# Optimization experiments

Hardware: AMD Instinct MI355X
Metric: run time of the kernel (lower is better)

Reference implementation:

```python
import jax, jax.numpy as jnp
import numpy as np

B, T = 32, 64            # batch, max caption length
E = 14                   # encoded image grid
ENC_D, DEC_D, ATT_D = 2048, 512, 512
PATCH, CH = 32, 3
FLAT = PATCH * PATCH * CH   # 3072
EMB = 256
PAD = PATCH // 2 + PATCH // 4  # 24
IMG = 512


def setup_inputs() -> dict:
    key = jax.random.key(0)
    ks = jax.random.split(key, 20)
    w = lambda k, shp: (0.02 * jax.random.normal(k, shp)).astype(jnp.float32)
    z = lambda *shp: jnp.zeros(shp, jnp.float32)
    lengths = jnp.concatenate(
        [jnp.array([[T]], jnp.int32),
         jax.random.randint(ks[4], (B - 1, 1), 1, T + 1, dtype=jnp.int32)], axis=0)
    return dict(
        encoder_out=jax.random.normal(ks[0], (B, E, E, ENC_D), jnp.float32),
        imgs=jax.random.normal(ks[1], (B, CH, IMG, IMG), jnp.float32),
        sequence=jax.random.randint(ks[2], (B, T, 2), 0, IMG - PATCH, dtype=jnp.int32),
        sequence_offset=jax.random.normal(ks[3], (B, T, 2), jnp.float32),
        caption_lengths=lengths,
        W_pe=w(ks[5], (EMB, FLAT)), b_pe=z(EMB),
        W_enc_att=w(ks[6], (ATT_D, ENC_D)), b_enc_att=z(ATT_D),
        W_dec_att=w(ks[7], (ATT_D, DEC_D)), b_dec_att=z(ATT_D),
        w_full=w(ks[8], (ATT_D,)), b_full=jnp.zeros((), jnp.float32),
        W_init_h=w(ks[9], (DEC_D, ENC_D + EMB)), b_init_h=z(DEC_D),
        W_init_c=w(ks[10], (DEC_D, ENC_D + EMB)), b_init_c=z(DEC_D),
        W_fb=w(ks[11], (ENC_D, DEC_D)), b_fb=z(ENC_D),
        W_ih=w(ks[12], (4 * DEC_D, ENC_D + EMB)), b_ih=z(4 * DEC_D),
        W_hh=w(ks[13], (4 * DEC_D, DEC_D)), b_hh=z(4 * DEC_D),
        W_fc=w(ks[14], (2, DEC_D)), b_fc=z(2),
        W_stop=w(ks[15], (1, DEC_D)), b_stop=z(1),
    )


def _extract_patches(imgs, seq):
    # imgs: [B,C,H,W] int keypoints seq: [B,T,2] (x,y); deterministic shift=0
    padded = jnp.pad(imgs, ((0, 0), (0, 0), (PAD, PAD), (PAD, PAD)))
    def one(img, kp):
        return jax.lax.dynamic_slice(img, (0, kp[1], kp[0]), (CH, PATCH, PATCH))
    return jax.vmap(lambda img, kps: jax.vmap(lambda kp: one(img, kp))(kps))(padded, seq)


def reference(encoder_out, imgs, sequence, sequence_offset, caption_lengths,
              W_pe, b_pe, W_enc_att, b_enc_att, W_dec_att, b_dec_att, w_full, b_full,
              W_init_h, b_init_h, W_init_c, b_init_c, W_fb, b_fb,
              W_ih, b_ih, W_hh, b_hh, W_fc, b_fc, W_stop, b_stop):
    lengths = caption_lengths[:, 0]
    sort_ind = jnp.argsort(-lengths)            # descending, like torch sort
    lengths = lengths[sort_ind]
    enc = encoder_out[sort_ind].reshape(B, -1, ENC_D)   # [B,P,ENC_D]
    imgs_s = imgs[sort_ind]
    seq_s = sequence[sort_ind]
    seq_off_s = sequence_offset[sort_ind]

    # patch embedding (dropout is identity in eval mode)
    patches = _extract_patches(imgs_s, seq_s).reshape(B, T, FLAT)
    emb = patches @ W_pe.T + b_pe               # [B,T,EMB]

    # init hidden state
    init_in = jnp.concatenate([enc.mean(axis=1), emb[:, 0, :]], axis=1)
    h = init_in @ W_init_h.T + b_init_h
    c = init_in @ W_init_c.T + b_init_c

    att1 = enc @ W_enc_att.T + b_enc_att        # [B,P,A] (loop-invariant)

    def step(carry, xs):
        h, c = carry
        emb_t, t = xs
        att2 = h @ W_dec_att.T + b_dec_att                       # [B,A]
        scores = jnp.einsum('bpa,a->bp', jax.nn.relu(att1 + att2[:, None, :]), w_full) + b_full
        alpha = jax.nn.softmax(scores, axis=1)                   # [B,P]
        awe = jnp.einsum('bpd,bp->bd', enc, alpha)               # [B,ENC_D]
        gate = jax.nn.sigmoid(h @ W_fb.T + b_fb)
        x = jnp.concatenate([gate * awe, emb_t], axis=1)
        gates = x @ W_ih.T + b_ih + h @ W_hh.T + b_hh
        i, f, g, o = jnp.split(gates, 4, axis=1)
        c_new = jax.nn.sigmoid(f) * c + jax.nn.sigmoid(i) * jnp.tanh(g)
        h_new = jax.nn.sigmoid(o) * jnp.tanh(c_new)
        mask = (t < lengths)[:, None]
        preds = jnp.where(mask, h_new @ W_fc.T + b_fc, 0.0)
        preds_stop = jnp.where(mask, jax.nn.sigmoid(h_new @ W_stop.T + b_stop), 0.0)
        alpha_m = jnp.where(mask, alpha, 0.0)
        h = jnp.where(mask, h_new, h)
        c = jnp.where(mask, c_new, c)
        return (h, c), (preds, preds_stop, alpha_m)

    (_, _), (P, PS, AL) = jax.lax.scan(step, (h, c), (emb.transpose(1, 0, 2), jnp.arange(T)))
    predictions = P.transpose(1, 0, 2)          # [B,T,2]
    predictions_stop = PS.transpose(1, 0, 2)    # [B,T,1]
    alphas = AL.transpose(1, 0, 2)              # [B,T,P]
    return predictions, predictions_stop, seq_off_s, lengths, alphas, sort_ind
```

## Files before the change

### kernel.cpp

```cpp
#include <hip/hip_runtime.h>

#define Bn 32
#define Tn 64
#define Pn 196
#define ENCD 2048
#define DECD 512
#define XDIM 2304

typedef unsigned short u16;
typedef __attribute__((ext_vector_type(8))) short bf16x8;
typedef __attribute__((ext_vector_type(4))) float f32x4;

#define MF(a,b,c) __builtin_amdgcn_mfma_f32_16x16x32_bf16(a,b,c,0,0,0)

static __device__ __forceinline__ u16 f2bf(float f){
  unsigned int u = __float_as_uint(f);
  unsigned int r = u + 0x7FFFu + ((u >> 16) & 1u);
  return (u16)(r >> 16);
}
static __device__ __forceinline__ float bf2f(u16 u){
  return __uint_as_float(((unsigned int)u) << 16);
}

#define O_PRED   0
#define O_STOP   4096
#define O_SEQOFF 6144
#define O_LEN    10240
#define O_ALPHA  10272
#define O_SORT   411680

#define WS_SORT    0
#define WS_LEN     32
#define WS_C       64
#define WS_PA      16448
#define WS_SCP     163904
#define WS_ENCM    215104
#define WS_EMB0    280640
#define WS_BCOMB   288832
#define US_H0      800000
#define US_H1      816384
#define US_XA      832768
#define US_EMBBF   898304
#define US_ATT1T   1422592
#define US_ENC     4830464
#define US_WAP     17675520
#define US_WIHE    20067584
#define US_WIH2    20591872
#define US_GEMB    24786176
#define US_PATCH   20591872
#define US_WPEB    26883328
#define US_WEA     27931904

__global__ void k_prep(const int* __restrict__ caplen, int* __restrict__ ws_sort,
                       int* __restrict__ ws_len, float* __restrict__ out){
  __shared__ int len[32];
  int i = threadIdx.x;
  if (i < 32) len[i] = caplen[i];
  __syncthreads();
  if (i < 32){
    int li = len[i], r = 0;
    for (int j = 0; j < 32; j++){
      int lj = len[j];
      r += (lj > li) || (lj == li && j < i);
    }
    ws_sort[r] = i;
    ws_len[r]  = li;
    out[O_LEN + r]  = (float)li;
    out[O_SORT + r] = (float)i;
  }
}

__global__ void k_seqoff(const float* __restrict__ seqoff, const int* __restrict__ ws_sort,
                         float* __restrict__ out){
  int idx = blockIdx.x*256 + threadIdx.x;
  int b = idx >> 7, r = idx & 127;
  out[O_SEQOFF + idx] = seqoff[ws_sort[b]*128 + r];
}

__global__ void k_encbf(const float* __restrict__ enc, const int* __restrict__ srt,
                        u16* __restrict__ dst){
  int m = blockIdx.x;
  int b = m / 196, p = m - b*196;
  const float* src = enc + ((size_t)srt[b]*196 + p)*ENCD;
  u16* d = dst + (size_t)m*ENCD;
  int i = threadIdx.x*8;
  float4 v0 = *(const float4*)(src + i);
  float4 v1 = *(const float4*)(src + i + 4);
  bf16x8 s;
  s[0]=(short)f2bf(v0.x); s[1]=(short)f2bf(v0.y); s[2]=(short)f2bf(v0.z); s[3]=(short)f2bf(v0.w);
  s[4]=(short)f2bf(v1.x); s[5]=(short)f2bf(v1.y); s[6]=(short)f2bf(v1.z); s[7]=(short)f2bf(v1.w);
  *(bf16x8*)(d + i) = s;
}

__global__ void k_encmean(const u16* __restrict__ encbf, float* __restrict__ encm){
  int b = blockIdx.x >> 3, dc = blockIdx.x & 7;
  int d = dc*256 + threadIdx.x;
  const u16* ep = encbf + (size_t)(b*196)*ENCD + d;
  float s = 0.f;
  #pragma unroll 4
  for (int p = 0; p < Pn; p++) s += bf2f(ep[(size_t)p*ENCD]);
  encm[b*ENCD + d] = s * (1.f/196.f);
}

__global__ void k_patch(const float* __restrict__ imgs, const int* __restrict__ seq,
                        const int* __restrict__ srt, u16* __restrict__ patches){
  int blk = blockIdx.x; int b = blk>>6, t = blk&63;
  int sb = srt[b];
  int x0 = seq[(sb*64+t)*2 + 0], y0 = seq[(sb*64+t)*2 + 1];
  const float* img = imgs + (size_t)sb*3*512*512;
  u16* dst = patches + (size_t)(b*64+t)*3072;
  for (int idx = threadIdx.x; idx < 3072; idx += 256){
    int c = idx>>10, rem = idx&1023, i = rem>>5, j = rem&31;
    int yy = y0 + i - 24, xx = x0 + j - 24;
    float v = 0.f;
    if ((unsigned)yy < 512u && (unsigned)xx < 512u) v = img[((size_t)c*512 + yy)*512 + xx];
    dst[idx] = f2bf(v);
  }
}

__global__ __launch_bounds__(256) void k_embedv3(const u16* __restrict__ patches,
    const u16* __restrict__ wpeb, const float* __restrict__ b_pe,
    u16* __restrict__ embbf, float* __restrict__ emb0){
  int mb = blockIdx.x >> 2, nb = blockIdx.x & 3;
  int m0 = mb*64;
  __shared__ u16 A[64*136];
  int tid = threadIdx.x, wv = tid>>6, lane = tid&63, lr = lane&15, lh = lane>>4;
  f32x4 acc[4];
  #pragma unroll
  for (int mt = 0; mt < 4; mt++) acc[mt] = (f32x4){0,0,0,0};
  for (int kc = 0; kc < 24; kc++){
    __syncthreads();
    {
      int row = tid>>2, seg = tid&3;
      const u16* src = patches + (size_t)(m0 + row)*3072 + kc*128 + seg*32;
      #pragma unroll
      for (int i = 0; i < 4; i++)
        *(bf16x8*)&A[row*136 + seg*32 + i*8] = *(const bf16x8*)(src + i*8);
    }
    __syncthreads();
    #pragma unroll
    for (int ki = 0; ki < 4; ki++){
      bf16x8 bv = *(const bf16x8*)&wpeb[(size_t)(nb*64 + wv*16 + lr)*3072 + kc*128 + ki*32 + lh*8];
      #pragma unroll
      for (int mt = 0; mt < 4; mt++){
        bf16x8 av = *(const bf16x8*)&A[(mt*16 + lr)*136 + ki*32 + lh*8];
        acc[mt] = MF(av, bv, acc[mt]);
      }
    }
  }
  int n = nb*64 + wv*16 + lr;
  float bias = b_pe[n];
  #pragma unroll
  for (int mt = 0; mt < 4; mt++){
    #pragma unroll
    for (int r = 0; r < 4; r++){
      int t = mt*16 + lh*4 + r;
      float val = acc[mt][r] + bias;
      embbf[(size_t)(m0 + t)*256 + n] = f2bf(val);
      if (t == 0) emb0[mb*256 + n] = val;
    }
  }
}

__global__ void k_cvt2(const float* __restrict__ Wih, const float* __restrict__ Whh,
    const float* __restrict__ Wdec, const float* __restrict__ Wfb,
    const float* __restrict__ Wfc, const float* __restrict__ Wstop,
    const float* __restrict__ Wea, const float* __restrict__ W_pe,
    const float* __restrict__ bih, const float* __restrict__ bhh,
    u16* __restrict__ WIH2, u16* __restrict__ WIHE,
    u16* __restrict__ WAP, u16* __restrict__ WEAd, u16* __restrict__ wpeb,
    float* __restrict__ bcomb){
  int blk = blockIdx.x, tid = threadIdx.x;
  if (blk < 2048){
    int r = blk, jp = (r & 511)*4 + (r >> 9);
    for (int i = tid; i < 2304; i += 256){
      u16 v = f2bf(Wih[(size_t)r*2304 + i]);
      if (i < 2048) WIH2[(size_t)jp*2048 + i] = v;
      else          WIHE[(size_t)jp*256 + (i - 2048)] = v;
    }
  } else if (blk < 6720){
    int j = blk - 2048;
    const float* src;
    if (j < 512)        src = Wdec + (size_t)j*512;
    else if (j < 2560)  src = Wfb + (size_t)(j-512)*512;
    else if (j < 4608)  src = Whh + (size_t)(j-2560)*512;
    else if (j == 4608) src = Wfc;
    else if (j == 4609) src = Wfc + 512;
    else if (j == 4610) src = Wstop;
    else src = 0;
    for (int i = tid; i < 512; i += 256)
      WAP[(size_t)j*512 + i] = src ? f2bf(src[i]) : (u16)0;
  } else if (blk < 7232){
    int r = blk - 6720;
    for (int i = tid; i < 2048; i += 256)
      WEAd[(size_t)r*2048 + i] = f2bf(Wea[(size_t)r*2048 + i]);
  } else if (blk < 7240){
    int jp = (blk - 7232)*256 + tid;
    int r = (jp & 3)*512 + (jp >> 2);
    bcomb[jp] = bih[r] + bhh[r];
  } else {
    int i = ((blk - 7240)*256 + tid)*4;
    float4 v = *(const float4*)(W_pe + i);
    wpeb[i+0] = f2bf(v.x); wpeb[i+1] = f2bf(v.y);
    wpeb[i+2] = f2bf(v.z); wpeb[i+3] = f2bf(v.w);
  }
}

__global__ __launch_bounds__(256) void k_gemb(const u16* __restrict__ embbf,
    const u16* __restrict__ WIHE, u16* __restrict__ gemb){
  int m0 = (blockIdx.x >> 3)*64, n0 = (blockIdx.x & 7)*256;
  __shared__ u16 A[64*264];
  int tid = threadIdx.x, wv = tid>>6, lane = tid&63, lr = lane&15, lh = lane>>4;
  {
    int row = tid>>2, seg = tid&3;
    const u16* src = embbf + (size_t)(m0 + row)*256 + seg*64;
    #pragma unroll
    for (int i = 0; i < 8; i++)
      *(bf16x8*)&A[row*264 + seg*64 + i*8] = *(const bf16x8*)(src + i*8);
  }
  __syncthreads();
  f32x4 acc[4][4];
  #pragma unroll
  for (int mt = 0; mt < 4; mt++)
    #pragma unroll
    for (int nt = 0; nt < 4; nt++) acc[mt][nt] = (f32x4){0,0,0,0};
  #pragma unroll
  for (int ki = 0; ki < 8; ki++){
    bf16x8 av[4];
    #pragma unroll
    for (int mt = 0; mt < 4; mt++)
      av[mt] = *(const bf16x8*)&A[(mt*16 + lr)*264 + ki*32 + lh*8];
    #pragma unroll
    for (int nt = 0; nt < 4; nt++){
      bf16x8 bv = *(const bf16x8*)&WIHE[(size_t)(n0 + wv*64 + nt*16 + lr)*256 + ki*32 + lh*8];
      #pragma unroll
      for (int mt = 0; mt < 4; mt++) acc[mt][nt] = MF(av[mt], bv, acc[mt][nt]);
    }
  }
  #pragma unroll
  for (int nt = 0; nt < 4; nt++){
    int n = n0 + wv*64 + nt*16 + lr;
    #pragma unroll
    for (int mt = 0; mt < 4; mt++)
      #pragma unroll
      for (int r = 0; r < 4; r++)
        gemb[(size_t)(m0 + mt*16 + lh*4 + r)*2048 + n] = f2bf(acc[mt][nt][r]);
  }
}

__global__ __launch_bounds__(256) void k_att1v4(const u16* __restrict__ encbf,
    const u16* __restrict__ Wea, const float* __restrict__ bea, u16* __restrict__ att1T){
  int mb = blockIdx.x >> 2, nb = blockIdx.x & 3;
  int m0 = mb*64;
  __shared__ u16 A[64*136];
  int tid = threadIdx.x, wv = tid>>6, lane = tid&63, lr = lane&15, lh = lane>>4;
  f32x4 acc[4][2];
  #pragma unroll
  for (int mt = 0; mt < 4; mt++){ acc[mt][0] = (f32x4){0,0,0,0}; acc[mt][1] = (f32x4){0,0,0,0}; }
  for (int kc = 0; kc < 16; kc++){
    __syncthreads();
    {
      int row = tid>>2, seg = tid&3;
      const u16* src = encbf + (size_t)(m0 + row)*2048 + kc*128 + seg*32;
      #pragma unroll
      for (int i = 0; i < 4; i++)
        *(bf16x8*)&A[row*136 + seg*32 + i*8] = *(const bf16x8*)(src + i*8);
    }
    __syncthreads();
    #pragma unroll
    for (int ki = 0; ki < 4; ki++){
      bf16x8 av[4];
      #pragma unroll
      for (int mt = 0; mt < 4; mt++)
        av[mt] = *(const bf16x8*)&A[(mt*16 + lr)*136 + ki*32 + lh*8];
      #pragma unroll
      for (int nt = 0; nt < 2; nt++){
        const u16* wp = Wea + (size_t)(nb*128 + wv*32 + nt*16 + lr)*2048 + kc*128 + ki*32 + lh*8;
        bf16x8 bv = *(const bf16x8*)wp;
        #pragma unroll
        for (int mt = 0; mt < 4; mt++) acc[mt][nt] = MF(av[mt], bv, acc[mt][nt]);
      }
    }
  }
  #pragma unroll
  for (int nt = 0; nt < 2; nt++){
    int n = nb*128 + wv*32 + nt*16 + lr;
    float bias = bea[n];
    #pragma unroll
    for (int mt = 0; mt < 4; mt++){
      #pragma unroll
      for (int r = 0; r < 4; r++){
        int m = m0 + mt*16 + lh*4 + r;
        int bb = m / 196, pp = m - bb*196;
        att1T[((size_t)bb*512 + n)*208 + pp] = f2bf(acc[mt][nt][r] + bias);
      }
    }
  }
}

__global__ __launch_bounds__(256) void k_initv3(const float* __restrict__ encm,
    const float* __restrict__ emb0,
    const float* __restrict__ Wh, const float* __restrict__ Wc,
    float* __restrict__ part){
  int kc = blockIdx.x >> 4, jb = blockIdx.x & 15;
  int tid = threadIdx.x, wv = tid>>6, lane = tid&63, lr = lane&15, lh = lane>>4;
  int j = jb*64 + wv*16 + lr;
  const float* wbase = (j < 512) ? (Wh + (size_t)j*XDIM) : (Wc + (size_t)(j-512)*XDIM);
  f32x4 acc0 = {0,0,0,0}, acc1 = {0,0,0,0};
  #pragma unroll 2
  for (int kk = 0; kk < 576; kk += 32){
    int k = kc*576 + kk + lh*8;
    float4 w0 = *(const float4*)(wbase + k);
    float4 w1 = *(const float4*)(wbase + k + 4);
    bf16x8 bv;
    bv[0]=(short)f2bf(w0.x); bv[1]=(short)f2bf(w0.y); bv[2]=(short)f2bf(w0.z); bv[3]=(short)f2bf(w0.w);
    bv[4]=(short)f2bf(w1.x); bv[5]=(short)f2bf(w1.y); bv[6]=(short)f2bf(w1.z); bv[7]=(short)f2bf(w1.w);
    float4 x0, x1, y0, y1;
    if (k < 2048){
      x0 = *(const float4*)(encm + (size_t)lr*2048 + k);
      x1 = *(const float4*)(encm + (size_t)lr*2048 + k + 4);
      y0 = *(const float4*)(encm + (size_t)(16+lr)*2048 + k);
      y1 = *(const float4*)(encm + (size_t)(16+lr)*2048 + k + 4);
    } else {
      int ke = k - 2048;
      x0 = *(const float4*)(emb0 + (size_t)lr*256 + ke);
      x1 = *(const float4*)(emb0 + (size_t)lr*256 + ke + 4);
      y0 = *(const float4*)(emb0 + (size_t)(16+lr)*256 + ke);
      y1 = *(const float4*)(emb0 + (size_t)(16+lr)*256 + ke + 4);
    }
    bf16x8 a0, a1;
    a0[0]=(short)f2bf(x0.x); a0[1]=(short)f2bf(x0.y); a0[2]=(short)f2bf(x0.z); a0[3]=(short)f2bf(x0.w);
    a0[4]=(short)f2bf(x1.x); a0[5]=(short)f2bf(x1.y); a0[6]=(short)f2bf(x1.z); a0[7]=(short)f2bf(x1.w);
    a1[0]=(short)f2bf(y0.x); a1[1]=(short)f2bf(y0.y); a1[2]=(short)f2bf(y0.z); a1[3]=(short)f2bf(y0.w);
    a1[4]=(short)f2bf(y1.x); a1[5]=(short)f2bf(y1.y); a1[6]=(short)f2bf(y1.z); a1[7]=(short)f2bf(y1.w);
    acc0 = MF(a0, bv, acc0);
    acc1 = MF(a1, bv, acc1);
  }
  #pragma unroll
  for (int r = 0; r < 4; ++r){
    int b0 = lh*4 + r, b1 = 16 + b0;
    part[(size_t)(kc*32 + b0)*1024 + j] = acc0[r];
    part[(size_t)(kc*32 + b1)*1024 + j] = acc1[r];
  }
}

__global__ __launch_bounds__(256) void k_initv3r(const float* __restrict__ part,
    const float* __restrict__ bh, const float* __restrict__ bc,
    u16* __restrict__ h_bf, float* __restrict__ c){
  int idx = blockIdx.x*256 + threadIdx.x;
  int b = idx >> 10, j = idx & 1023;
  float s = part[(size_t)b*1024 + j] + part[(size_t)(32+b)*1024 + j]
          + part[(size_t)(64+b)*1024 + j] + part[(size_t)(96+b)*1024 + j];
  if (j < 512) h_bf[(size_t)b*512 + j] = f2bf(s + bh[j]);
  else         c[(size_t)b*512 + (j-512)] = s + bc[j-512];
}

__global__ __launch_bounds__(256) void kAB(const u16* __restrict__ h, const u16* __restrict__ WAP,
    float* __restrict__ pA, const u16* __restrict__ att1T,
    const float* __restrict__ bdec, const float* __restrict__ wfull,
    float* __restrict__ scp, const float* __restrict__ bfc, const float* __restrict__ bstop,
    const int* __restrict__ len, float* __restrict__ out, int t){
  int blk = blockIdx.x, tid = threadIdx.x;
  if (t == 64 && blk != 64) return;
  if (blk < 65){
    __shared__ u16 HL[32*520];
    int wv = tid>>6, lane = tid&63, lr = lane&15, lh = lane>>4;
    for (int i = tid; i < 4096; i += 256){
      unsigned long long v = ((const unsigned long long*)h)[i];
      int row = i >> 7, col = (i & 127)*4;
      *(unsigned long long*)&HL[row*520 + col] = v;
    }
    __syncthreads();
    int j0 = 512 + blk*64 + wv*16;
    f32x4 acc0 = {0,0,0,0}, acc1 = {0,0,0,0};
    #pragma unroll 4
    for (int ki = 0; ki < 16; ++ki){
      bf16x8 bv = *(const bf16x8*)&WAP[(size_t)(j0+lr)*512 + ki*32 + lh*8];
      bf16x8 a0 = *(const bf16x8*)&HL[lr*520 + ki*32 + lh*8];
      bf16x8 a1 = *(const bf16x8*)&HL[(16+lr)*520 + ki*32 + lh*8];
      acc0 = MF(a0, bv, acc0);
      acc1 = MF(a1, bv, acc1);
    }
    int j = j0 + lr;
    if (j < 4608){
      #pragma unroll
      for (int r = 0; r < 4; ++r){
        pA[(size_t)(lh*4+r)*4608 + j]    = acc0[r];
        pA[(size_t)(lh*4+r+16)*4608 + j] = acc1[r];
      }
    } else if (j < 4611 && t > 0){
      int jj = j - 4608, tm1 = t - 1;
      #pragma unroll
      for (int r = 0; r < 4; ++r){
        #pragma unroll
        for (int hb = 0; hb < 2; ++hb){
          int b0 = lh*4 + r + hb*16;
          float val = hb ? acc1[r] : acc0[r];
          bool mk = tm1 < len[b0];
          if (jj < 2) out[O_PRED + ((size_t)b0*64 + tm1)*2 + jj] = mk ? val + bfc[jj] : 0.f;
          else        out[O_STOP + (size_t)b0*64 + tm1] =
                        mk ? 1.f/(1.f + expf(-(val + bstop[0]))) : 0.f;
        }
      }
    }
  } else {
    int kb = blk - 65, b = kb >> 3, ac = kb & 7;
    if (t >= len[b]) return;
    __shared__ u16 hL[512];
    __shared__ float a2s[64], wfs[64];
    if (tid < 128)
      ((unsigned long long*)hL)[tid] = ((const unsigned long long*)(h + (size_t)b*512))[tid];
    if (tid < 64) wfs[tid] = wfull[ac*64 + tid];
    __syncthreads();
    {
      int a = tid >> 2, q = tid & 3;
      const u16* wrow = WAP + (size_t)(ac*64 + a)*512 + q*128;
      const u16* hrow = hL + q*128;
      float acc = 0.f;
      #pragma unroll
      for (int i = 0; i < 16; ++i){
        bf16x8 wv8 = *(const bf16x8*)(wrow + i*8);
        bf16x8 hv8 = *(const bf16x8*)(hrow + i*8);
        #pragma unroll
        for (int e = 0; e < 8; ++e) acc += bf2f((u16)hv8[e]) * bf2f((u16)wv8[e]);
      }
      acc += __shfl_xor(acc, 1);
      acc += __shfl_xor(acc, 2);
      if (q == 0) a2s[a] = acc + bdec[ac*64 + a];
    }
    __syncthreads();
    int p = tid;
    if (p < 196){
      const u16* col = att1T + ((size_t)b*512 + ac*64)*208 + p;
      float acc = 0.f;
      #pragma unroll 8
      for (int a = 0; a < 64; ++a)
        acc += fmaxf(bf2f(col[(size_t)a*208]) + a2s[a], 0.f) * wfs[a];
      scp[(size_t)(b*8 + ac)*200 + p] = acc;
    }
  }
}

__global__ __launch_bounds__(256) void kB2(const float* __restrict__ scp,
    const float* __restrict__ pA, const u16* __restrict__ encbf,
    const float* __restrict__ bfull, const float* __restrict__ bfb,
    u16* __restrict__ xa, const int* __restrict__ len, float* __restrict__ out, int t){
  int b = blockIdx.x >> 3, dc = blockIdx.x & 7;
  int tid = threadIdx.x, wv = tid>>6, lane = tid&63;
  if (t >= len[b]){
    if (dc == 0 && tid < 196) out[O_ALPHA + ((size_t)b*64 + t)*196 + tid] = 0.f;
    return;
  }
  __shared__ float ev[200], redf[4], bcx[2];
  float s = -1e30f;
  if (tid < 196){
    s = bfull[0];
    #pragma unroll
    for (int q = 0; q < 8; ++q) s += scp[(size_t)(b*8 + q)*200 + tid];
  }
  float m = s;
  #pragma unroll
  for (int o = 32; o; o >>= 1) m = fmaxf(m, __shfl_down(m, o));
  if (lane == 0) redf[wv] = m;
  __syncthreads();
  if (tid == 0) bcx[0] = fmaxf(fmaxf(redf[0],redf[1]), fmaxf(redf[2],redf[3]));
  __syncthreads();
  float e = (tid < 196) ? expf(s - bcx[0]) : 0.f;
  if (tid < 200) ev[tid] = (tid < 196) ? e : 0.f;
  float sm = e;
  #pragma unroll
  for (int o = 32; o; o >>= 1) sm += __shfl_down(sm, o);
  __syncthreads();
  if (lane == 0) redf[wv] = sm;
  __syncthreads();
  if (tid == 0) bcx[1] = redf[0]+redf[1]+redf[2]+redf[3];
  __syncthreads();
  float ssum = bcx[1];
  int d = dc*256 + tid;
  const u16* ep = encbf + (size_t)(b*196)*ENCD + d;
  float q[8];
  #pragma unroll
  for (int j = 0; j < 8; ++j) q[j] = 0.f;
  #pragma unroll 2
  for (int p = 0; p < 192; p += 8){
    #pragma unroll
    for (int j = 0; j < 8; ++j)
      q[j] += ev[p+j]*bf2f(ep[(size_t)(p+j)*ENCD]);
  }
  #pragma unroll
  for (int j = 0; j < 4; ++j)
    q[j] += ev[192+j]*bf2f(ep[(size_t)(192+j)*ENCD]);
  float awe = (((q[0]+q[1])+(q[2]+q[3])) + ((q[4]+q[5])+(q[6]+q[7]))) / ssum;
  float gp = pA[(size_t)b*4608 + 512 + d] + bfb[d];
  float gate = 1.f/(1.f + expf(-gp));
  xa[(size_t)b*2048 + d] = f2bf(gate * awe);
  if (dc == 0 && tid < 196) out[O_ALPHA + ((size_t)b*64 + t)*196 + tid] = ev[tid]/ssum;
}

__global__ __launch_bounds__(512) void kC(const u16* __restrict__ xa,
    const u16* __restrict__ hc, u16* __restrict__ hn, float* __restrict__ c,
    const u16* __restrict__ WIH2, const float* __restrict__ pA,
    const float* __restrict__ bcomb, const u16* __restrict__ gemb,
    const int* __restrict__ len, int t){
  int tid = threadIdx.x, wv = tid>>6, lane = tid&63, lr = lane&15, lh = lane>>4;
  int jp0 = blockIdx.x*16;
  __shared__ float red[8*512];
  f32x4 acc0 = {0,0,0,0}, acc1 = {0,0,0,0};
  #pragma unroll
  for (int ks = 0; ks < 8; ++ks){
    int k = wv*256 + ks*32;
    bf16x8 a0 = *(const bf16x8*)&xa[(size_t)lr*2048 + k + lh*8];
    bf16x8 a1 = *(const bf16x8*)&xa[(size_t)(16+lr)*2048 + k + lh*8];
    bf16x8 bv = *(const bf16x8*)&WIH2[(size_t)(jp0+lr)*2048 + k + lh*8];
    acc0 = MF(a0, bv, acc0);
    acc1 = MF(a1, bv, acc1);
  }
  #pragma unroll
  for (int r = 0; r < 4; ++r){
    red[wv*512 + ((lh*4+r) << 4) + lr]    = acc0[r];
    red[wv*512 + ((16+lh*4+r) << 4) + lr] = acc1[r];
  }
  __syncthreads();
  {
    int b = tid >> 4, jl = tid & 15, e = jl & 3;
    int jp = jp0 + jl, u = jp >> 2;
    float g = 0.f;
    #pragma unroll
    for (int w = 0; w < 8; ++w) g += red[w*512 + tid];
    g += bcomb[jp] + bf2f(gemb[((size_t)b*64 + t)*2048 + jp])
       + pA[(size_t)b*4608 + 2560 + e*512 + u];
    float sv = (e == 2) ? tanhf(g) : 1.f/(1.f + expf(-g));
    float vb = __shfl_xor(sv, 1), vc = __shfl_xor(sv, 2), vd = __shfl_xor(vb, 2);
    float i_s = (e==0)?sv:(e==1)?vb:(e==2)?vc:vd;
    float f_s = (e==1)?sv:(e==0)?vb:(e==3)?vc:vd;
    float g_t = (e==2)?sv:(e==3)?vb:(e==0)?vc:vd;
    float o_s = (e==3)?sv:(e==2)?vb:(e==1)?vc:vd;
    float cold = c[(size_t)b*512 + u];
    float hold = bf2f(hc[(size_t)b*512 + u]);
    bool mk = t < len[b];
    float cn = mk ? (f_s*cold + i_s*g_t) : cold;
    float hv = mk ? (o_s * tanhf(cn)) : hold;
    if (e == 0){
      c[(size_t)b*512 + u] = cn;
      hn[(size_t)b*512 + u] = f2bf(hv);
    }
  }
}

extern "C" void kernel_launch(void* const* d_in, const int* in_sizes, int n_in,
                              void* d_out, int out_size, void* d_ws, size_t ws_size,
                              hipStream_t stream){
  (void)in_sizes; (void)n_in; (void)out_size; (void)ws_size;
  const float* enc_out   = (const float*)d_in[0];
  const float* imgs      = (const float*)d_in[1];
  const int*   seq       = (const int*)d_in[2];
  const float* seqoff    = (const float*)d_in[3];
  const int*   caplen    = (const int*)d_in[4];
  const float* W_pe      = (const float*)d_in[5];
  const float* b_pe      = (const float*)d_in[6];
  const float* W_enc_att = (const float*)d_in[7];
  const float* b_enc_att = (const float*)d_in[8];
  const float* W_dec_att = (const float*)d_in[9];
  const float* b_dec_att = (const float*)d_in[10];
  const float* w_full    = (const float*)d_in[11];
  const float* b_full    = (const float*)d_in[12];
  const float* W_init_h  = (const float*)d_in[13];
  const float* b_init_h  = (const float*)d_in[14];
  const float* W_init_c  = (const float*)d_in[15];
  const float* b_init_c  = (const float*)d_in[16];
  const float* W_fb      = (const float*)d_in[17];
  const float* b_fb      = (const float*)d_in[18];
  const float* W_ih      = (const float*)d_in[19];
  const float* b_ih      = (const float*)d_in[20];
  const float* W_hh      = (const float*)d_in[21];
  const float* b_hh      = (const float*)d_in[22];
  const float* W_fc      = (const float*)d_in[23];
  const float* b_fc      = (const float*)d_in[24];
  const float* W_stop    = (const float*)d_in[25];
  const float* b_stop    = (const float*)d_in[26];

  float* out = (float*)d_out;
  float* ws  = (float*)d_ws;
  int*   wsi = (int*)d_ws;
  u16*   us  = (u16*)d_ws;

  u16* H[2] = { us + US_H0, us + US_H1 };

  k_prep<<<1, 64, 0, stream>>>(caplen, wsi + WS_SORT, wsi + WS_LEN, out);
  k_seqoff<<<16, 256, 0, stream>>>(seqoff, wsi + WS_SORT, out);
  k_encbf<<<6272, 256, 0, stream>>>(enc_out, wsi + WS_SORT, us + US_ENC);
  k_encmean<<<256, 256, 0, stream>>>(us + US_ENC, ws + WS_ENCM);
  k_patch<<<2048, 256, 0, stream>>>(imgs, seq, wsi + WS_SORT, us + US_PATCH);
  k_cvt2<<<8008, 256, 0, stream>>>(W_ih, W_hh, W_dec_att, W_fb, W_fc, W_stop, W_enc_att, W_pe,
                                   b_ih, b_hh,
                                   us + US_WIH2, us + US_WIHE, us + US_WAP,
                                   us + US_WEA, us + US_WPEB, ws + WS_BCOMB);
  k_embedv3<<<128, 256, 0, stream>>>(us + US_PATCH, us + US_WPEB, b_pe,
                                     us + US_EMBBF, ws + WS_EMB0);
  k_att1v4<<<392, 256, 0, stream>>>(us + US_ENC, us + US_WEA, b_enc_att, us + US_ATT1T);
  k_gemb<<<256, 256, 0, stream>>>(us + US_EMBBF, us + US_WIHE, us + US_GEMB);
  k_initv3<<<64, 256, 0, stream>>>(ws + WS_ENCM, ws + WS_EMB0, W_init_h, W_init_c, ws + WS_PA);
  k_initv3r<<<128, 256, 0, stream>>>(ws + WS_PA, b_init_h, b_init_c, H[0], ws + WS_C);

  for (int t = 0; t < Tn; ++t){
    kAB<<<321, 256, 0, stream>>>(H[t & 1], us + US_WAP, ws + WS_PA, us + US_ATT1T,
                                 b_dec_att, w_full, ws + WS_SCP, b_fc, b_stop,
                                 wsi + WS_LEN, out, t);
    kB2<<<256, 256, 0, stream>>>(ws + WS_SCP, ws + WS_PA, us + US_ENC, b_full, b_fb,
                                 us + US_XA, wsi + WS_LEN, out, t);
    kC<<<128, 512, 0, stream>>>(us + US_XA, H[t & 1], H[(t + 1) & 1], ws + WS_C,
                                us + US_WIH2, ws + WS_PA, ws + WS_BCOMB, us + US_GEMB,
                                wsi + WS_LEN, t);
  }
  kAB<<<321, 256, 0, stream>>>(H[0], us + US_WAP, ws + WS_PA, us + US_ATT1T,
                               b_dec_att, w_full, ws + WS_SCP, b_fc, b_stop,
                               wsi + WS_LEN, out, 64);
}
```

Before: 1.919 ms.

## Merge prologue kernels into four dependency-staged launches

Combines the ten setup kernels (sort-gather, bf16 conversions, patch extraction, encoder mean, patch embedding, attention projection, input gate GEMM, and init h/c) into four launches. Each launch groups independent work by block index. The encoder mean now reads the fp32 encoder output directly instead of the bf16 copy, so it no longer has to wait for the conversion. The goal is less launch overhead and more concurrent work in the one-time prologue, while the 64-step recurrent loop stays unchanged. Mixing heterogeneous branches in one grid can unbalance block scheduling, and the encoder mean changes slightly numerically because it now sums fp32 rather than bf16 values.

New measurement: 1.904 ms. Within noise of the previous version (-0.8%).

```diff
diff --git a/kernel.cpp b/kernel.cpp
--- a/kernel.cpp
+++ b/kernel.cpp
@@ -70,106 +70,168 @@
   }
 }
 
-__global__ void k_seqoff(const float* __restrict__ seqoff, const int* __restrict__ ws_sort,
-                         float* __restrict__ out){
-  int idx = blockIdx.x*256 + threadIdx.x;
-  int b = idx >> 7, r = idx & 127;
-  out[O_SEQOFF + idx] = seqoff[ws_sort[b]*128 + r];
-}
-
-__global__ void k_encbf(const float* __restrict__ enc, const int* __restrict__ srt,
-                        u16* __restrict__ dst){
-  int m = blockIdx.x;
-  int b = m / 196, p = m - b*196;
-  const float* src = enc + ((size_t)srt[b]*196 + p)*ENCD;
-  u16* d = dst + (size_t)m*ENCD;
-  int i = threadIdx.x*8;
-  float4 v0 = *(const float4*)(src + i);
-  float4 v1 = *(const float4*)(src + i + 4);
-  bf16x8 s;
-  s[0]=(short)f2bf(v0.x); s[1]=(short)f2bf(v0.y); s[2]=(short)f2bf(v0.z); s[3]=(short)f2bf(v0.w);
-  s[4]=(short)f2bf(v1.x); s[5]=(short)f2bf(v1.y); s[6]=(short)f2bf(v1.z); s[7]=(short)f2bf(v1.w);
-  *(bf16x8*)(d + i) = s;
-}
-
-__global__ void k_encmean(const u16* __restrict__ encbf, float* __restrict__ encm){
-  int b = blockIdx.x >> 3, dc = blockIdx.x & 7;
-  int d = dc*256 + threadIdx.x;
-  const u16* ep = encbf + (size_t)(b*196)*ENCD + d;
-  float s = 0.f;
-  #pragma unroll 4
-  for (int p = 0; p < Pn; p++) s += bf2f(ep[(size_t)p*ENCD]);
-  encm[b*ENCD + d] = s * (1.f/196.f);
-}
-
-__global__ void k_patch(const float* __restrict__ imgs, const int* __restrict__ seq,
-                        const int* __restrict__ srt, u16* __restrict__ patches){
-  int blk = blockIdx.x; int b = blk>>6, t = blk&63;
-  int sb = srt[b];
-  int x0 = seq[(sb*64+t)*2 + 0], y0 = seq[(sb*64+t)*2 + 1];
-  const float* img = imgs + (size_t)sb*3*512*512;
-  u16* dst = patches + (size_t)(b*64+t)*3072;
-  for (int idx = threadIdx.x; idx < 3072; idx += 256){
-    int c = idx>>10, rem = idx&1023, i = rem>>5, j = rem&31;
-    int yy = y0 + i - 24, xx = x0 + j - 24;
-    float v = 0.f;
-    if ((unsigned)yy < 512u && (unsigned)xx < 512u) v = img[((size_t)c*512 + yy)*512 + xx];
-    dst[idx] = f2bf(v);
-  }
-}
-
-__global__ __launch_bounds__(256) void k_embedv3(const u16* __restrict__ patches,
+__global__ __launch_bounds__(256) void k_stageA(const float* __restrict__ enc,
+    const float* __restrict__ imgs, const int* __restrict__ seq,
+    const float* __restrict__ W_pe, const float* __restrict__ Wea,
+    const float* __restrict__ seqoff, const int* __restrict__ srt,
+    u16* __restrict__ encbf, float* __restrict__ encm, u16* __restrict__ patches,
+    u16* __restrict__ wpeb, u16* __restrict__ wead, float* __restrict__ out){
+  int blk = blockIdx.x, tid = threadIdx.x;
+  if (blk < 6272){
+    int m = blk;
+    int b = m / 196, p = m - b*196;
+    const float* src = enc + ((size_t)srt[b]*196 + p)*ENCD;
+    u16* d = encbf + (size_t)m*ENCD;
+    int i = tid*8;
+    float4 v0 = *(const float4*)(src + i);
+    float4 v1 = *(const float4*)(src + i + 4);
+    bf16x8 s;
+    s[0]=(short)f2bf(v0.x); s[1]=(short)f2bf(v0.y); s[2]=(short)f2bf(v0.z); s[3]=(short)f2bf(v0.w);
+    s[4]=(short)f2bf(v1.x); s[5]=(short)f2bf(v1.y); s[6]=(short)f2bf(v1.z); s[7]=(short)f2bf(v1.w);
+    *(bf16x8*)(d + i) = s;
+  } else if (blk < 6528){
+    int r = blk - 6272;
+    int b = r >> 3, dc = r & 7;
+    int d = dc*256 + tid;
+    const float* ep = enc + ((size_t)srt[b]*196)*ENCD + d;
+    float s = 0.f;
+    #pragma unroll 4
+    for (int p = 0; p < Pn; p++) s += ep[(size_t)p*ENCD];
+    encm[b*ENCD + d] = s * (1.f/196.f);
+  } else if (blk < 8576){
+    int r = blk - 6528;
+    int b = r>>6, t = r&63;
+    int sb = srt[b];
+    int x0 = seq[(sb*64+t)*2 + 0], y0 = seq[(sb*64+t)*2 + 1];
+    const float* img = imgs + (size_t)sb*3*512*512;
+    u16* dst = patches + (size_t)(b*64+t)*3072;
+    for (int idx = tid; idx < 3072; idx += 256){
+      int c = idx>>10, rem = idx&1023, i = rem>>5, j = rem&31;
+      int yy = y0 + i - 24, xx = x0 + j - 24;
+      float v = 0.f;
+      if ((unsigned)yy < 512u && (unsigned)xx < 512u) v = img[((size_t)c*512 + yy)*512 + xx];
+      dst[idx] = f2bf(v);
+    }
+  } else if (blk < 9344){
+    int i = ((blk - 8576)*256 + tid)*4;
+    float4 v = *(const float4*)(W_pe + i);
+    wpeb[i+0] = f2bf(v.x); wpeb[i+1] = f2bf(v.y);
+    wpeb[i+2] = f2bf(v.z); wpeb[i+3] = f2bf(v.w);
+  } else if (blk < 9856){
+    int r = blk - 9344;
+    for (int i = tid; i < 2048; i += 256)
+      wead[(size_t)r*2048 + i] = f2bf(Wea[(size_t)r*2048 + i]);
+  } else {
+    int idx = (blk - 9856)*256 + tid;
+    int b = idx >> 7, r = idx & 127;
+    out[O_SEQOFF + idx] = seqoff[srt[b]*128 + r];
+  }
+}
+
+__global__ __launch_bounds__(256) void k_stageB(const u16* __restrict__ patches,
     const u16* __restrict__ wpeb, const float* __restrict__ b_pe,
-    u16* __restrict__ embbf, float* __restrict__ emb0){
-  int mb = blockIdx.x >> 2, nb = blockIdx.x & 3;
-  int m0 = mb*64;
+    const u16* __restrict__ encbf, const u16* __restrict__ wead,
+    const float* __restrict__ bea,
+    u16* __restrict__ embbf, float* __restrict__ emb0, u16* __restrict__ att1T){
   __shared__ u16 A[64*136];
-  int tid = threadIdx.x, wv = tid>>6, lane = tid&63, lr = lane&15, lh = lane>>4;
-  f32x4 acc[4];
-  #pragma unroll
-  for (int mt = 0; mt < 4; mt++) acc[mt] = (f32x4){0,0,0,0};
-  for (int kc = 0; kc < 24; kc++){
-    __syncthreads();
-    {
-      int row = tid>>2, seg = tid&3;
-      const u16* src = patches + (size_t)(m0 + row)*3072 + kc*128 + seg*32;
-      #pragma unroll
-      for (int i = 0; i < 4; i++)
-        *(bf16x8*)&A[row*136 + seg*32 + i*8] = *(const bf16x8*)(src + i*8);
-    }
-    __syncthreads();
-    #pragma unroll
-    for (int ki = 0; ki < 4; ki++){
-      bf16x8 bv = *(const bf16x8*)&wpeb[(size_t)(nb*64 + wv*16 + lr)*3072 + kc*128 + ki*32 + lh*8];
+  int blk = blockIdx.x, tid = threadIdx.x;
+  int wv = tid>>6, lane = tid&63, lr = lane&15, lh = lane>>4;
+  if (blk < 128){
+    int mb = blk >> 2, nb = blk & 3;
+    int m0 = mb*64;
+    f32x4 acc[4];
+    #pragma unroll
+    for (int mt = 0; mt < 4; mt++) acc[mt] = (f32x4){0,0,0,0};
+    for (int kc = 0; kc < 24; kc++){
+      __syncthreads();
+      {
+        int row = tid>>2, seg = tid&3;
+        const u16* src = patches + (size_t)(m0 + row)*3072 + kc*128 + seg*32;
+        #pragma unroll
+        for (int i = 0; i < 4; i++)
+          *(bf16x8*)&A[row*136 + seg*32 + i*8] = *(const bf16x8*)(src + i*8);
+      }
+      __syncthreads();
+      #pragma unroll
+      for (int ki = 0; ki < 4; ki++){
+        bf16x8 bv = *(const bf16x8*)&wpeb[(size_t)(nb*64 + wv*16 + lr)*3072 + kc*128 + ki*32 + lh*8];
+        #pragma unroll
+        for (int mt = 0; mt < 4; mt++){
+          bf16x8 av = *(const bf16x8*)&A[(mt*16 + lr)*136 + ki*32 + lh*8];
+          acc[mt] = MF(av, bv, acc[mt]);
+        }
+      }
+    }
+    int n = nb*64 + wv*16 + lr;
+    float bias = b_pe[n];
+    #pragma unroll
+    for (int mt = 0; mt < 4; mt++){
+      #pragma unroll
+      for (int r = 0; r < 4; r++){
+        int t = mt*16 + lh*4 + r;
+        float val = acc[mt][r] + bias;
+        embbf[(size_t)(m0 + t)*256 + n] = f2bf(val);
+        if (t == 0) emb0[mb*256 + n] = val;
+      }
+    }
+  } else {
+    int ab = blk - 128;
+    int mb = ab >> 2, nb = ab & 3;
+    int m0 = mb*64;
+    f32x4 acc[4][2];
+    #pragma unroll
+    for (int mt = 0; mt < 4; mt++){ acc[mt][0] = (f32x4){0,0,0,0}; acc[mt][1] = (f32x4){0,0,0,0}; }
+    for (int kc = 0; kc < 16; kc++){
+      __syncthreads();
+      {
+        int row = tid>>2, seg = tid&3;
+        const u16* src = encbf + (size_t)(m0 + row)*2048 + kc*128 + seg*32;
+        #pragma unroll
+        for (int i = 0; i < 4; i++)
+          *(bf16x8*)&A[row*136 + seg*32 + i*8] = *(const bf16x8*)(src + i*8);
+      }
+      __syncthreads();
+      #pragma unroll
+      for (int ki = 0; ki < 4; ki++){
+        bf16x8 av[4];
+        #pragma unroll
+        for (int mt = 0; mt < 4; mt++)
+          av[mt] = *(const bf16x8*)&A[(mt*16 + lr)*136 + ki*32 + lh*8];
+        #pragma unroll
+        for (int nt = 0; nt < 2; nt++){
+          const u16* wp = wead + (size_t)(nb*128 + wv*32 + nt*16 + lr)*2048 + kc*128 + ki*32 + lh*8;
+          bf16x8 bv = *(const bf16x8*)wp;
+          #pragma unroll
+          for (int mt = 0; mt < 4; mt++) acc[mt][nt] = MF(av[mt], bv, acc[mt][nt]);
+        }
+      }
+    }
+    #pragma unroll
+    for (int nt = 0; nt < 2; nt++){
+      int n = nb*128 + wv*32 + nt*16 + lr;
+      float bias = bea[n];
       #pragma unroll
       for (int mt = 0; mt < 4; mt++){
-        bf16x8 av = *(const bf16x8*)&A[(mt*16 + lr)*136 + ki*32 + lh*8];
-        acc[mt] = MF(av, bv, acc[mt]);
-      }
-    }
-  }
-  int n = nb*64 + wv*16 + lr;
-  float bias = b_pe[n];
-  #pragma unroll
-  for (int mt = 0; mt < 4; mt++){
-    #pragma unroll
-    for (int r = 0; r < 4; r++){
-      int t = mt*16 + lh*4 + r;
-      float val = acc[mt][r] + bias;
-      embbf[(size_t)(m0 + t)*256 + n] = f2bf(val);
-      if (t == 0) emb0[mb*256 + n] = val;
-    }
-  }
-}
-
-__global__ void k_cvt2(const float* __restrict__ Wih, const float* __restrict__ Whh,
-    const float* __restrict__ Wdec, const float* __restrict__ Wfb,
-    const float* __restrict__ Wfc, const float* __restrict__ Wstop,
-    const float* __restrict__ Wea, const float* __restrict__ W_pe,
-    const float* __restrict__ bih, const float* __restrict__ bhh,
-    u16* __restrict__ WIH2, u16* __restrict__ WIHE,
-    u16* __restrict__ WAP, u16* __restrict__ WEAd, u16* __restrict__ wpeb,
-    float* __restrict__ bcomb){
+        #pragma unroll
+        for (int r = 0; r < 4; r++){
+          int m = m0 + mt*16 + lh*4 + r;
+          int bb = m / 196, pp = m - bb*196;
+          att1T[((size_t)bb*512 + n)*208 + pp] = f2bf(acc[mt][nt][r] + bias);
+        }
+      }
+    }
+  }
+}
+
+__global__ __launch_bounds__(256) void k_stageC(const float* __restrict__ Wih,
+    const float* __restrict__ Whh, const float* __restrict__ Wdec,
+    const float* __restrict__ Wfb, const float* __restrict__ Wfc,
+    const float* __restrict__ Wstop, const float* __restrict__ bih,
+    const float* __restrict__ bhh,
+    const float* __restrict__ encm, const float* __restrict__ emb0,
+    const float* __restrict__ Wh, const float* __restrict__ Wc,
+    u16* __restrict__ WIH2, u16* __restrict__ WIHE, u16* __restrict__ WAP,
+    float* __restrict__ bcomb, float* __restrict__ part){
   int blk = blockIdx.x, tid = threadIdx.x;
   if (blk < 2048){
     int r = blk, jp = (r & 511)*4 + (r >> 9);
@@ -190,169 +252,107 @@
     else src = 0;
     for (int i = tid; i < 512; i += 256)
       WAP[(size_t)j*512 + i] = src ? f2bf(src[i]) : (u16)0;
-  } else if (blk < 7232){
-    int r = blk - 6720;
-    for (int i = tid; i < 2048; i += 256)
-      WEAd[(size_t)r*2048 + i] = f2bf(Wea[(size_t)r*2048 + i]);
-  } else if (blk < 7240){
-    int jp = (blk - 7232)*256 + tid;
+  } else if (blk < 6728){
+    int jp = (blk - 6720)*256 + tid;
     int r = (jp & 3)*512 + (jp >> 2);
     bcomb[jp] = bih[r] + bhh[r];
   } else {
-    int i = ((blk - 7240)*256 + tid)*4;
-    float4 v = *(const float4*)(W_pe + i);
-    wpeb[i+0] = f2bf(v.x); wpeb[i+1] = f2bf(v.y);
-    wpeb[i+2] = f2bf(v.z); wpeb[i+3] = f2bf(v.w);
-  }
-}
-
-__global__ __launch_bounds__(256) void k_gemb(const u16* __restrict__ embbf,
-    const u16* __restrict__ WIHE, u16* __restrict__ gemb){
-  int m0 = (blockIdx.x >> 3)*64, n0 = (blockIdx.x & 7)*256;
+    int ib = blk - 6728;
+    int kc = ib >> 4, jb = ib & 15;
+    int wv = tid>>6, lane = tid&63, lr = lane&15, lh = lane>>4;
+    int j = jb*64 + wv*16 + lr;
+    const float* wbase = (j < 512) ? (Wh + (size_t)j*XDIM) : (Wc + (size_t)(j-512)*XDIM);
+    f32x4 acc0 = {0,0,0,0}, acc1 = {0,0,0,0};
+    #pragma unroll 2
+    for (int kk = 0; kk < 576; kk += 32){
+      int k = kc*576 + kk + lh*8;
+      float4 w0 = *(const float4*)(wbase + k);
+      float4 w1 = *(const float4*)(wbase + k + 4);
+      bf16x8 bv;
+      bv[0]=(short)f2bf(w0.x); bv[1]=(short)f2bf(w0.y); bv[2]=(short)f2bf(w0.z); bv[3]=(short)f2bf(w0.w);
+      bv[4]=(short)f2bf(w1.x); bv[5]=(short)f2bf(w1.y); bv[6]=(short)f2bf(w1.z); bv[7]=(short)f2bf(w1.w);
+      float4 x0, x1, y0, y1;
+      if (k < 2048){
+        x0 = *(const float4*)(encm + (size_t)lr*2048 + k);
+        x1 = *(const float4*)(encm + (size_t)lr*2048 + k + 4);
+        y0 = *(const float4*)(encm + (size_t)(16+lr)*2048 + k);
+        y1 = *(const float4*)(encm + (size_t)(16+lr)*2048 + k + 4);
+      } else {
+        int ke = k - 2048;
+        x0 = *(const float4*)(emb0 + (size_t)lr*256 + ke);
+        x1 = *(const float4*)(emb0 + (size_t)lr*256 + ke + 4);
+        y0 = *(const float4*)(emb0 + (size_t)(16+lr)*256 + ke);
+        y1 = *(const float4*)(emb0 + (size_t)(16+lr)*256 + ke + 4);
+      }
+      bf16x8 a0, a1;
+      a0[0]=(short)f2bf(x0.x); a0[1]=(short)f2bf(x0.y); a0[2]=(short)f2bf(x0.z); a0[3]=(short)f2bf(x0.w);
+      a0[4]=(short)f2bf(x1.x); a0[5]=(short)f2bf(x1.y); a0[6]=(short)f2bf(x1.z); a0[7]=(short)f2bf(x1.w);
+      a1[0]=(short)f2bf(y0.x); a1[1]=(short)f2bf(y0.y); a1[2]=(short)f2bf(y0.z); a1[3]=(short)f2bf(y0.w);
+      a1[4]=(short)f2bf(y1.x); a1[5]=(short)f2bf(y1.y); a1[6]=(short)f2bf(y1.z); a1[7]=(short)f2bf(y1.w);
+      acc0 = MF(a0, bv, acc0);
+      acc1 = MF(a1, bv, acc1);
+    }
+    #pragma unroll
+    for (int r = 0; r < 4; ++r){
+      int b0 = lh*4 + r, b1 = 16 + b0;
+      part[(size_t)(kc*32 + b0)*1024 + j] = acc0[r];
+      part[(size_t)(kc*32 + b1)*1024 + j] = acc1[r];
+    }
+  }
+}
+
+__global__ __launch_bounds__(256) void k_stageD(const u16* __restrict__ embbf,
+    const u16* __restrict__ WIHE, const float* __restrict__ part,
+    const float* __restrict__ bh, const float* __restrict__ bc,
+    u16* __restrict__ gemb, u16* __restrict__ h_bf, float* __restrict__ c){
   __shared__ u16 A[64*264];
-  int tid = threadIdx.x, wv = tid>>6, lane = tid&63, lr = lane&15, lh = lane>>4;
-  {
-    int row = tid>>2, seg = tid&3;
-    const u16* src = embbf + (size_t)(m0 + row)*256 + seg*64;
-    #pragma unroll
-    for (int i = 0; i < 8; i++)
-      *(bf16x8*)&A[row*264 + seg*64 + i*8] = *(const bf16x8*)(src + i*8);
-  }
-  __syncthreads();
-  f32x4 acc[4][4];
-  #pragma unroll
-  for (int mt = 0; mt < 4; mt++)
-    #pragma unroll
-    for (int nt = 0; nt < 4; nt++) acc[mt][nt] = (f32x4){0,0,0,0};
-  #pragma unroll
-  for (int ki = 0; ki < 8; ki++){
-    bf16x8 av[4];
-    #pragma unroll
-    for (int mt = 0; mt < 4; mt++)
-      av[mt] = *(const bf16x8*)&A[(mt*16 + lr)*264 + ki*32 + lh*8];
-    #pragma unroll
-    for (int nt = 0; nt < 4; nt++){
-      bf16x8 bv = *(const bf16x8*)&WIHE[(size_t)(n0 + wv*64 + nt*16 + lr)*256 + ki*32 + lh*8];
-      #pragma unroll
-      for (int mt = 0; mt < 4; mt++) acc[mt][nt] = MF(av[mt], bv, acc[mt][nt]);
-    }
-  }
-  #pragma unroll
-  for (int nt = 0; nt < 4; nt++){
-    int n = n0 + wv*64 + nt*16 + lr;
-    #pragma unroll
-    for (int mt = 0; mt < 4; mt++)
-      #pragma unroll
-      for (int r = 0; r < 4; r++)
-        gemb[(size_t)(m0 + mt*16 + lh*4 + r)*2048 + n] = f2bf(acc[mt][nt][r]);
-  }
-}
-
-__global__ __launch_bounds__(256) void k_att1v4(const u16* __restrict__ encbf,
-    const u16* __restrict__ Wea, const float* __restrict__ bea, u16* __restrict__ att1T){
-  int mb = blockIdx.x >> 2, nb = blockIdx.x & 3;
-  int m0 = mb*64;
-  __shared__ u16 A[64*136];
-  int tid = threadIdx.x, wv = tid>>6, lane = tid&63, lr = lane&15, lh = lane>>4;
-  f32x4 acc[4][2];
-  #pragma unroll
-  for (int mt = 0; mt < 4; mt++){ acc[mt][0] = (f32x4){0,0,0,0}; acc[mt][1] = (f32x4){0,0,0,0}; }
-  for (int kc = 0; kc < 16; kc++){
-    __syncthreads();
+  int blk = blockIdx.x, tid = threadIdx.x;
+  if (blk < 256){
+    int m0 = (blk >> 3)*64, n0 = (blk & 7)*256;
+    int wv = tid>>6, lane = tid&63, lr = lane&15, lh = lane>>4;
     {
       int row = tid>>2, seg = tid&3;
-      const u16* src = encbf + (size_t)(m0 + row)*2048 + kc*128 + seg*32;
-      #pragma unroll
-      for (int i = 0; i < 4; i++)
-        *(bf16x8*)&A[row*136 + seg*32 + i*8] = *(const bf16x8*)(src + i*8);
+      const u16* src = embbf + (size_t)(m0 + row)*256 + seg*64;
+      #pragma unroll
+      for (int i = 0; i < 8; i++)
+        *(bf16x8*)&A[row*264 + seg*64 + i*8] = *(const bf16x8*)(src + i*8);
     }
     __syncthreads();
-    #pragma unroll
-    for (int ki = 0; ki < 4; ki++){
+    f32x4 acc[4][4];
+    #pragma unroll
+    for (int mt = 0; mt < 4; mt++)
+      #pragma unroll
+      for (int nt = 0; nt < 4; nt++) acc[mt][nt] = (f32x4){0,0,0,0};
+    #pragma unroll
+    for (int ki = 0; ki < 8; ki++){
       bf16x8 av[4];
       #pragma unroll
       for (int mt = 0; mt < 4; mt++)
-        av[mt] = *(const bf16x8*)&A[(mt*16 + lr)*136 + ki*32 + lh*8];
-      #pragma unroll
-      for (int nt = 0; nt < 2; nt++){
-        const u16* wp = Wea + (size_t)(nb*128 + wv*32 + nt*16 + lr)*2048 + kc*128 + ki*32 + lh*8;
-        bf16x8 bv = *(const bf16x8*)wp;
+        av[mt] = *(const bf16x8*)&A[(mt*16 + lr)*264 + ki*32 + lh*8];
+      #pragma unroll
+      for (int nt = 0; nt < 4; nt++){
+        bf16x8 bv = *(const bf16x8*)&WIHE[(size_t)(n0 + wv*64 + nt*16 + lr)*256 + ki*32 + lh*8];
         #pragma unroll
         for (int mt = 0; mt < 4; mt++) acc[mt][nt] = MF(av[mt], bv, acc[mt][nt]);
       }
     }
-  }
-  #pragma unroll
-  for (int nt = 0; nt < 2; nt++){
-    int n = nb*128 + wv*32 + nt*16 + lr;
-    float bias = bea[n];
-    #pragma unroll
-    for (int mt = 0; mt < 4; mt++){
-      #pragma unroll
-      for (int r = 0; r < 4; r++){
-        int m = m0 + mt*16 + lh*4 + r;
-        int bb = m / 196, pp = m - bb*196;
-        att1T[((size_t)bb*512 + n)*208 + pp] = f2bf(acc[mt][nt][r] + bias);
-      }
-    }
-  }
-}
-
-__global__ __launch_bounds__(256) void k_initv3(const float* __restrict__ encm,
-    const float* __restrict__ emb0,
-    const float* __restrict__ Wh, const float* __restrict__ Wc,
-    float* __restrict__ part){
-  int kc = blockIdx.x >> 4, jb = blockIdx.x & 15;
-  int tid = threadIdx.x, wv = tid>>6, lane = tid&63, lr = lane&15, lh = lane>>4;
-  int j = jb*64 + wv*16 + lr;
-  const float* wbase = (j < 512) ? (Wh + (size_t)j*XDIM) : (Wc + (size_t)(j-512)*XDIM);
-  f32x4 acc0 = {0,0,0,0}, acc1 = {0,0,0,0};
-  #pragma unroll 2
-  for (int kk = 0; kk < 576; kk += 32){
-    int k = kc*576 + kk + lh*8;
-    float4 w0 = *(const float4*)(wbase + k);
-    float4 w1 = *(const float4*)(wbase + k + 4);
-    bf16x8 bv;
-    bv[0]=(short)f2bf(w0.x); bv[1]=(short)f2bf(w0.y); bv[2]=(short)f2bf(w0.z); bv[3]=(short)f2bf(w0.w);
-    bv[4]=(short)f2bf(w1.x); bv[5]=(short)f2bf(w1.y); bv[6]=(short)f2bf(w1.z); bv[7]=(short)f2bf(w1.w);
-    float4 x0, x1, y0, y1;
-    if (k < 2048){
-      x0 = *(const float4*)(encm + (size_t)lr*2048 + k);
-      x1 = *(const float4*)(encm + (size_t)lr*2048 + k + 4);
-      y0 = *(const float4*)(encm + (size_t)(16+lr)*2048 + k);
-      y1 = *(const float4*)(encm + (size_t)(16+lr)*2048 + k + 4);
-    } else {
-      int ke = k - 2048;
-      x0 = *(const float4*)(emb0 + (size_t)lr*256 + ke);
-      x1 = *(const float4*)(emb0 + (size_t)lr*256 + ke + 4);
-      y0 = *(const float4*)(emb0 + (size_t)(16+lr)*256 + ke);
-      y1 = *(const float4*)(emb0 + (size_t)(16+lr)*256 + ke + 4);
-    }
-    bf16x8 a0, a1;
-    a0[0]=(short)f2bf(x0.x); a0[1]=(short)f2bf(x0.y); a0[2]=(short)f2bf(x0.z); a0[3]=(short)f2bf(x0.w);
-    a0[4]=(short)f2bf(x1.x); a0[5]=(short)f2bf(x1.y); a0[6]=(short)f2bf(x1.z); a0[7]=(short)f2bf(x1.w);
-    a1[0]=(short)f2bf(y0.x); a1[1]=(short)f2bf(y0.y); a1[2]=(short)f2bf(y0.z); a1[3]=(short)f2bf(y0.w);
-    a1[4]=(short)f2bf(y1.x); a1[5]=(short)f2bf(y1.y); a1[6]=(short)f2bf(y1.z); a1[7]=(short)f2bf(y1.w);
-    acc0 = MF(a0, bv, acc0);
-    acc1 = MF(a1, bv, acc1);
-  }
-  #pragma unroll
-  for (int r = 0; r < 4; ++r){
-    int b0 = lh*4 + r, b1 = 16 + b0;
-    part[(size_t)(kc*32 + b0)*1024 + j] = acc0[r];
-    part[(size_t)(kc*32 + b1)*1024 + j] = acc1[r];
-  }
-}
-
-__global__ __launch_bounds__(256) void k_initv3r(const float* __restrict__ part,
-    const float* __restrict__ bh, const float* __restrict__ bc,
-    u16* __restrict__ h_bf, float* __restrict__ c){
-  int idx = blockIdx.x*256 + threadIdx.x;
-  int b = idx >> 10, j = idx & 1023;
-  float s = part[(size_t)b*1024 + j] + part[(size_t)(32+b)*1024 + j]
-          + part[(size_t)(64+b)*1024 + j] + part[(size_t)(96+b)*1024 + j];
-  if (j < 512) h_bf[(size_t)b*512 + j] = f2bf(s + bh[j]);
-  else         c[(size_t)b*512 + (j-512)] = s + bc[j-512];
+    #pragma unroll
+    for (int nt = 0; nt < 4; nt++){
+      int n = n0 + wv*64 + nt*16 + lr;
+      #pragma unroll
+      for (int mt = 0; mt < 4; mt++)
+        #pragma unroll
+        for (int r = 0; r < 4; r++)
+          gemb[(size_t)(m0 + mt*16 + lh*4 + r)*2048 + n] = f2bf(acc[mt][nt][r]);
+    }
+  } else {
+    int idx = (blk - 256)*256 + tid;
+    int b = idx >> 10, j = idx & 1023;
+    float s = part[(size_t)b*1024 + j] + part[(size_t)(32+b)*1024 + j]
+            + part[(size_t)(64+b)*1024 + j] + part[(size_t)(96+b)*1024 + j];
+    if (j < 512) h_bf[(size_t)b*512 + j] = f2bf(s + bh[j]);
+    else         c[(size_t)b*512 + (j-512)] = s + bc[j-512];
+  }
 }
 
 __global__ __launch_bounds__(256) void kAB(const u16* __restrict__ h, const u16* __restrict__ WAP,
@@ -587,20 +587,21 @@
   u16* H[2] = { us + US_H0, us + US_H1 };
 
   k_prep<<<1, 64, 0, stream>>>(caplen, wsi + WS_SORT, wsi + WS_LEN, out);
-  k_seqoff<<<16, 256, 0, stream>>>(seqoff, wsi + WS_SORT, out);
-  k_encbf<<<6272, 256, 0, stream>>>(enc_out, wsi + WS_SORT, us + US_ENC);
-  k_encmean<<<256, 256, 0, stream>>>(us + US_ENC, ws + WS_ENCM);
-  k_patch<<<2048, 256, 0, stream>>>(imgs, seq, wsi + WS_SORT, us + US_PATCH);
-  k_cvt2<<<8008, 256, 0, stream>>>(W_ih, W_hh, W_dec_att, W_fb, W_fc, W_stop, W_enc_att, W_pe,
-                                   b_ih, b_hh,
-                                   us + US_WIH2, us + US_WIHE, us + US_WAP,
-                                   us + US_WEA, us + US_WPEB, ws + WS_BCOMB);
-  k_embedv3<<<128, 256, 0, stream>>>(us + US_PATCH, us + US_WPEB, b_pe,
-                                     us + US_EMBBF, ws + WS_EMB0);
-  k_att1v4<<<392, 256, 0, stream>>>(us + US_ENC, us + US_WEA, b_enc_att, us + US_ATT1T);
-  k_gemb<<<256, 256, 0, stream>>>(us + US_EMBBF, us + US_WIHE, us + US_GEMB);
-  k_initv3<<<64, 256, 0, stream>>>(ws + WS_ENCM, ws + WS_EMB0, W_init_h, W_init_c, ws + WS_PA);
-  k_initv3r<<<128, 256, 0, stream>>>(ws + WS_PA, b_init_h, b_init_c, H[0], ws + WS_C);
+  k_stageA<<<9872, 256, 0, stream>>>(enc_out, imgs, seq, W_pe, W_enc_att, seqoff,
+                                     wsi + WS_SORT,
+                                     us + US_ENC, ws + WS_ENCM, us + US_PATCH,
+                                     us + US_WPEB, us + US_WEA, out);
+  k_stageB<<<520, 256, 0, stream>>>(us + US_PATCH, us + US_WPEB, b_pe,
+                                    us + US_ENC, us + US_WEA, b_enc_att,
+                                    us + US_EMBBF, ws + WS_EMB0, us + US_ATT1T);
+  k_stageC<<<6792, 256, 0, stream>>>(W_ih, W_hh, W_dec_att, W_fb, W_fc, W_stop,
+                                     b_ih, b_hh,
+                                     ws + WS_ENCM, ws + WS_EMB0, W_init_h, W_init_c,
+                                     us + US_WIH2, us + US_WIHE, us + US_WAP,
+                                     ws + WS_BCOMB, ws + WS_PA);
+  k_stageD<<<384, 256, 0, stream>>>(us + US_EMBBF, us + US_WIHE, ws + WS_PA,
+                                    b_init_h, b_init_c,
+                                    us + US_GEMB, H[0], ws + WS_C);
 
   for (int t = 0; t < Tn; ++t){
     kAB<<<321, 256, 0, stream>>>(H[t & 1], us + US_WAP, ws + WS_PA, us + US_ATT1T,
```
